# Kernel optimization log

Hardware: AMD Instinct MI355X
Metric: run time of the kernel (lower is better)

## Reference

```python
import jax, jax.numpy as jnp
import numpy as np

B, T, H = 16, 512, 384   # batch, phoneme length, hidden
F, K = 384, 3            # filter size, kernel size
DMAX = 8                 # max per-token duration
L = T * DMAX             # static max expanded length (original uses real_len.max())


def conv1d_same(x, w, b):
    # x: [B, T, Cin], w: [Cout, Cin, K] (torch OIW layout), padding = K//2 both sides
    y = jax.lax.conv_general_dilated(
        x.transpose(0, 2, 1), w, window_strides=(1,),
        padding=[(K // 2, K // 2)], dimension_numbers=('NCW', 'OIW', 'NCW'))
    return y.transpose(0, 2, 1) + b


def layer_norm(x, g, b, eps=1e-5):
    mu = jnp.mean(x, axis=-1, keepdims=True)
    var = jnp.mean(jnp.square(x - mu), axis=-1, keepdims=True)
    return (x - mu) * jax.lax.rsqrt(var + eps) * g + b


def setup_inputs() -> dict:
    key = jax.random.key(0)
    ks = jax.random.split(key, 10)
    x = jax.random.normal(ks[0], (B, T, H), dtype=jnp.float32)
    # log-durations whose exp().round() gives integers in [1, DMAX]
    dur = jax.random.randint(ks[1], (B, T), 1, DMAX + 1)
    true_durations = jnp.log(dur.astype(jnp.float32))
    s1 = 1.0 / np.sqrt(H * K)
    s2 = 1.0 / np.sqrt(F * K)
    s3 = 1.0 / np.sqrt(F)
    return {
        'x': x,
        'true_durations': true_durations,
        'conv1_w': jax.random.uniform(ks[2], (F, H, K), jnp.float32, -s1, s1),
        'conv1_b': jnp.zeros((F,), jnp.float32),
        'ln1_g': jnp.ones((F,), jnp.float32),
        'ln1_b': jnp.zeros((F,), jnp.float32),
        'conv2_w': jax.random.uniform(ks[3], (F, F, K), jnp.float32, -s2, s2),
        'conv2_b': jnp.zeros((F,), jnp.float32),
        'ln2_g': jnp.ones((F,), jnp.float32),
        'ln2_b': jnp.zeros((F,), jnp.float32),
        'lin_w': jax.random.uniform(ks[4], (F, 1), jnp.float32, -s3, s3),
        'lin_b': jnp.zeros((1,), jnp.float32),
    }


def reference(x, true_durations, conv1_w, conv1_b, ln1_g, ln1_b,
              conv2_w, conv2_b, ln2_g, ln2_b, lin_w, lin_b):
    # duration predictor net (dropout in eval mode = identity)
    h = conv1d_same(x, conv1_w, conv1_b)
    h = jax.nn.gelu(layer_norm(h, ln1_g, ln1_b), approximate=False)
    h = conv1d_same(h, conv2_w, conv2_b)
    h = jax.nn.gelu(layer_norm(h, ln2_g, ln2_b), approximate=False)
    length = jax.nn.relu(h @ lin_w + lin_b)[..., 0]  # [B, T]

    # length regulation with ground-truth durations (detached ints in original)
    dur = jnp.round(jnp.exp(true_durations)).astype(jnp.int32)  # [B, T]
    ends = jnp.cumsum(dur, axis=1)          # [B, T]
    starts = ends - dur                     # [B, T]
    k = jnp.arange(L)                       # [L]
    # binary alignment: A[b,t,l] = 1 iff starts[b,t] <= l < ends[b,t]
    A = ((k >= starts[..., None]) & (k < ends[..., None])).astype(x.dtype)  # [B,T,L]
    out = jnp.einsum('bth,btl->blh', x, A)  # = (x^T @ A)^T, [B, L, H]
    return out, length
```

## Files before the change

### kernel.cpp

```cpp
#include <hip/hip_runtime.h>
#include <stdint.h>

typedef unsigned short u16;
typedef unsigned int   u32;

#define B_    16
#define T_    512
#define H_    384
#define F_    384
#define DMAX_ 8
#define L_    4096
#define KD    1152
#define M_    8192

typedef __bf16 bf16x8 __attribute__((ext_vector_type(8)));
typedef float  f32x4  __attribute__((ext_vector_type(4)));

typedef __attribute__((address_space(1))) u32 gu32;
typedef __attribute__((address_space(3))) u32 lu32;

__device__ __forceinline__ void dma16(const void* g, void* l) {
    __builtin_amdgcn_global_load_lds((gu32*)(uintptr_t)g, (lu32*)(u32)(uintptr_t)l, 16, 0, 0);
}

__device__ __forceinline__ u16 f2b(float f) {
    union { float f; u32 i; } v; v.f = f;
    u32 x = v.i;
    return (u16)((x + 0x7fffu + ((x >> 16) & 1u)) >> 16);
}

__global__ void k_durmap(const float* __restrict__ td, int* __restrict__ tmap) {
    __shared__ int s[T_];
    int b = blockIdx.x, t = threadIdx.x;
    int d = (int)roundf(expf(td[b * T_ + t]));
    if (d < 0) d = 0; if (d > DMAX_) d = DMAX_;
    int v = d;
    s[t] = v;
    __syncthreads();
    for (int off = 1; off < T_; off <<= 1) {
        int add = (t >= off) ? s[t - off] : 0;
        __syncthreads();
        v += add;
        s[t] = v;
        __syncthreads();
    }
    int end = v, start = end - d;
    for (int i = start; i < end; ++i) tmap[b * L_ + i] = t;
    int total = s[T_ - 1];
    for (int l = total + t; l < L_; l += T_) tmap[b * L_ + l] = -1;
}

__global__ void k_expand(const float* __restrict__ x, const int* __restrict__ tmap,
                         float* __restrict__ out) {
    int v = blockIdx.x * blockDim.x + threadIdx.x;
    if (v >= B_ * L_ * 96) return;
    int row = v / 96, c4 = v % 96;
    int b = row >> 12;
    int t = tmap[row];
    uint4 val = make_uint4(0u, 0u, 0u, 0u);
    if (t >= 0) val = *(const uint4*)(x + (size_t)((b << 9) + t) * H_ + c4 * 4);
    *(uint4*)(out + (size_t)row * H_ + c4 * 4) = val;
}

__global__ void k_xcast(const float* __restrict__ x, u16* __restrict__ xb) {
    int v = blockIdx.x * blockDim.x + threadIdx.x;
    if (v >= M_ * 96) return;
    float4 f = *(const float4*)(x + (size_t)v * 4);
    u16 o[4] = { f2b(f.x), f2b(f.y), f2b(f.z), f2b(f.w) };
    *(uint2*)(xb + (size_t)v * 4) = *(uint2*)o;
}

__global__ void k_repack(const float* __restrict__ w1, const float* __restrict__ w2,
                         u16* __restrict__ Wp1, u16* __restrict__ Wp2,
                         u16* __restrict__ zp) {
    int i = blockIdx.x * blockDim.x + threadIdx.x;
    if (i < 128) zp[i] = 0;
    const int n = F_ * H_ * 3;
    if (i >= 2 * n) return;
    const float* src = (i < n) ? w1 : w2;
    u16* dst         = (i < n) ? Wp1 : Wp2;
    int j = (i < n) ? i : i - n;
    int f = j / (H_ * 3);
    int rem = j % (H_ * 3);
    int c = rem / 3, kk = rem % 3;
    dst[f * KD + kk * H_ + c] = f2b(src[j]);
}

__launch_bounds__(256, 4)
__global__ void k_gemm(const u16* __restrict__ src, const u16* __restrict__ Wp,
                       const float* __restrict__ bias, float* __restrict__ C,
                       const u16* __restrict__ zp) {
    __shared__ u16 smem[768 * 8];
    int tid = threadIdx.x;
    int w = tid >> 6, lane = tid & 63;
    int quad = lane >> 4, l16 = lane & 15;
    int m0 = blockIdx.x * 64;
    int n0 = blockIdx.y * 128;

    int idx0 = w * 64 + lane;
    int rowA = idx0 >> 2;
    int qA   = (idx0 & 3) ^ ((rowA >> 1) & 3);
    int arow = m0 + rowA;
    int bB   = arow >> 9, tt = arow & 511;
    int rowB = idx0 >> 2;
    int qB   = (idx0 & 3) ^ ((rowB >> 1) & 3);
    const u16* srcB1 = Wp + (size_t)(n0 + rowB) * KD + qB * 8;
    const u16* srcB2 = Wp + (size_t)(n0 + rowB + 64) * KD + qB * 8;
    u16* ldsA  = smem + (size_t)w * 512;
    u16* ldsB1 = smem + 2048 + (size_t)w * 512;
    u16* ldsB2 = smem + 4096 + (size_t)w * 512;

    int wm = w & 1, wn = w >> 1;
    const u16* aptr[2];
    const u16* bptr[4];
    #pragma unroll
    for (int i = 0; i < 2; ++i) {
        int row = wm * 32 + i * 16 + l16;
        aptr[i] = smem + (((row << 2) | (quad ^ ((row >> 1) & 3))) << 3);
    }
    #pragma unroll
    for (int j = 0; j < 4; ++j) {
        int row = wn * 64 + j * 16 + l16;
        bptr[j] = smem + ((256 + ((row << 2) | (quad ^ ((row >> 1) & 3)))) << 3);
    }

    f32x4 acc[2][4];
    #pragma unroll
    for (int i = 0; i < 2; ++i)
        #pragma unroll
        for (int j = 0; j < 4; ++j)
            acc[i][j] = f32x4{0.f, 0.f, 0.f, 0.f};

    for (int k0 = 0; k0 < KD; k0 += 32) {
        int kg = k0 + qA * 8;
        int kk = (kg >= 768) ? 2 : ((kg >= 384) ? 1 : 0);
        int c  = kg - kk * 384;
        int ts = tt + kk - 1;
        const u16* sA = (ts >= 0 && ts < T_) ? (src + (size_t)((bB << 9) + ts) * H_ + c) : zp;
        dma16(sA, ldsA);
        dma16(srcB1 + k0, ldsB1);
        dma16(srcB2 + k0, ldsB2);
        __syncthreads();

        bf16x8 af[2], bfr[4];
        #pragma unroll
        for (int i = 0; i < 2; ++i) af[i]  = *(const bf16x8*)aptr[i];
        #pragma unroll
        for (int j = 0; j < 4; ++j) bfr[j] = *(const bf16x8*)bptr[j];
        #pragma unroll
        for (int i = 0; i < 2; ++i)
            #pragma unroll
            for (int j = 0; j < 4; ++j)
                acc[i][j] = __builtin_amdgcn_mfma_f32_16x16x32_bf16(af[i], bfr[j], acc[i][j], 0, 0, 0);
        __syncthreads();
    }

    #pragma unroll
    for (int i = 0; i < 2; ++i) {
        #pragma unroll
        for (int j = 0; j < 4; ++j) {
            int row = m0 + wm * 32 + i * 16 + quad * 4;
            int col = n0 + wn * 64 + j * 16 + l16;
            float bb = bias[col];
            #pragma unroll
            for (int r = 0; r < 4; ++r)
                C[(size_t)(row + r) * F_ + col] = acc[i][j][r] + bb;
        }
    }
}

__global__ void k_lngelu(const float* __restrict__ Hin, const float* __restrict__ g,
                         const float* __restrict__ bta, u16* __restrict__ G) {
    int row = blockIdx.x;
    int lane = threadIdx.x;
    const float* hr = Hin + (size_t)row * F_;
    float vals[6];
    float s = 0.f, s2 = 0.f;
    #pragma unroll
    for (int j = 0; j < 6; ++j) {
        float xv = hr[lane + j * 64];
        vals[j] = xv; s += xv; s2 += xv * xv;
    }
    #pragma unroll
    for (int off = 32; off; off >>= 1) { s += __shfl_down(s, off); s2 += __shfl_down(s2, off); }
    s = __shfl(s, 0); s2 = __shfl(s2, 0);
    float mean = s * (1.f / F_);
    float var  = s2 * (1.f / F_) - mean * mean;
    float rstd = rsqrtf(var + 1e-5f);
    #pragma unroll
    for (int j = 0; j < 6; ++j) {
        int c = lane + j * 64;
        float y  = (vals[j] - mean) * rstd * g[c] + bta[c];
        float gl = 0.5f * y * (1.f + erff(y * 0.70710678118654752f));
        G[(size_t)row * F_ + c] = f2b(gl);
    }
}

__global__ void k_len(const float* __restrict__ Hin, const float* __restrict__ g,
                      const float* __restrict__ bta, const float* __restrict__ lw,
                      const float* __restrict__ lb, float* __restrict__ lenout) {
    int row = blockIdx.x;
    int lane = threadIdx.x;
    const float* hr = Hin + (size_t)row * F_;
    float vals[6];
    float s = 0.f, s2 = 0.f;
    #pragma unroll
    for (int j = 0; j < 6; ++j) {
        float xv = hr[lane + j * 64];
        vals[j] = xv; s += xv; s2 += xv * xv;
    }
    #pragma unroll
    for (int off = 32; off; off >>= 1) { s += __shfl_down(s, off); s2 += __shfl_down(s2, off); }
    s = __shfl(s, 0); s2 = __shfl(s2, 0);
    float mean = s * (1.f / F_);
    float var  = s2 * (1.f / F_) - mean * mean;
    float rstd = rsqrtf(var + 1e-5f);
    float dot = 0.f;
    #pragma unroll
    for (int j = 0; j < 6; ++j) {
        int c = lane + j * 64;
        float y  = (vals[j] - mean) * rstd * g[c] + bta[c];
        float gl = 0.5f * y * (1.f + erff(y * 0.70710678118654752f));
        dot += gl * lw[c];
    }
    #pragma unroll
    for (int off = 32; off; off >>= 1) dot += __shfl_down(dot, off);
    if (lane == 0) {
        float r = dot + lb[0];
        lenout[row] = fmaxf(r, 0.f);
    }
}

extern "C" void kernel_launch(void* const* d_in, const int* in_sizes, int n_in,
                              void* d_out, int out_size, void* d_ws, size_t ws_size,
                              hipStream_t stream) {
    const float* x   = (const float*)d_in[0];
    const float* td  = (const float*)d_in[1];
    const float* w1  = (const float*)d_in[2];
    const float* b1  = (const float*)d_in[3];
    const float* g1  = (const float*)d_in[4];
    const float* be1 = (const float*)d_in[5];
    const float* w2  = (const float*)d_in[6];
    const float* b2  = (const float*)d_in[7];
    const float* g2  = (const float*)d_in[8];
    const float* be2 = (const float*)d_in[9];
    const float* lw  = (const float*)d_in[10];
    const float* lb  = (const float*)d_in[11];

    float* out0 = (float*)d_out;
    float* out1 = out0 + (size_t)B_ * L_ * H_;

    char* ws = (char*)d_ws;
    size_t off = 0;
    auto carve = [&](size_t bytes) -> void* {
        void* p = ws + off;
        off = (off + bytes + 255) & ~(size_t)255;
        return p;
    };
    int*  tmap  = (int*)carve((size_t)B_ * L_ * sizeof(int));
    u16*  Wp1   = (u16*)carve((size_t)F_ * KD * sizeof(u16));
    u16*  Wp2   = (u16*)carve((size_t)F_ * KD * sizeof(u16));
    u16*  xb    = (u16*)carve((size_t)M_ * H_ * sizeof(u16));
    u16*  G     = (u16*)carve((size_t)M_ * F_ * sizeof(u16));
    u16*  zp    = (u16*)carve(256);
    float* Hbuf = (float*)carve((size_t)M_ * F_ * sizeof(float));

    k_durmap<<<B_, T_, 0, stream>>>(td, tmap);
    k_expand<<<(B_ * L_ * 96 + 255) / 256, 256, 0, stream>>>(x, tmap, out0);

    k_repack<<<(2 * F_ * H_ * 3 + 255) / 256, 256, 0, stream>>>(w1, w2, Wp1, Wp2, zp);
    k_xcast<<<(M_ * 96 + 255) / 256, 256, 0, stream>>>(x, xb);
    k_gemm<<<dim3(M_ / 64, 3), 256, 0, stream>>>(xb, Wp1, b1, Hbuf, zp);
    k_lngelu<<<M_, 64, 0, stream>>>(Hbuf, g1, be1, G);
    k_gemm<<<dim3(M_ / 64, 3), 256, 0, stream>>>(G, Wp2, b2, Hbuf, zp);
    k_len<<<M_, 64, 0, stream>>>(Hbuf, g2, be2, lw, lb, out1);
}
```

Baseline: 212.0 us.

## Retile conv GEMM to 32x128 with K=64 steps and store bf16 intermediates

The conv GEMM moves from 64x128 tiles with K=32 steps to 32x128 tiles with K=64 steps. This halves the number of barrier pairs and doubles MFMA work per sync, and the grid doubles to 768 blocks. The A-row gather now precomputes three tap base pointers instead of branching per step. The GEMM output is stored as bf16 rather than fp32, halving intermediate traffic into the LayerNorm kernels at the cost of an extra rounding before normalization.

After: 197.9 us. 6.7% less time.

```diff
diff --git a/kernel.cpp b/kernel.cpp
--- a/kernel.cpp
+++ b/kernel.cpp
@@ -27,6 +27,9 @@
     union { float f; u32 i; } v; v.f = f;
     u32 x = v.i;
     return (u16)((x + 0x7fffu + ((x >> 16) & 1u)) >> 16);
+}
+__device__ __forceinline__ float b2f(u16 u) {
+    union { u32 i; float f; } v; v.i = ((u32)u) << 16; return v.f;
 }
 
 __global__ void k_durmap(const float* __restrict__ td, int* __restrict__ tmap) {
@@ -74,7 +77,7 @@
                          u16* __restrict__ Wp1, u16* __restrict__ Wp2,
                          u16* __restrict__ zp) {
     int i = blockIdx.x * blockDim.x + threadIdx.x;
-    if (i < 128) zp[i] = 0;
+    if (i < 512) zp[i] = 0;
     const int n = F_ * H_ * 3;
     if (i >= 2 * n) return;
     const float* src = (i < n) ? w1 : w2;
@@ -86,99 +89,119 @@
     dst[f * KD + kk * H_ + c] = f2b(src[j]);
 }
 
-__launch_bounds__(256, 4)
+__launch_bounds__(256, 3)
 __global__ void k_gemm(const u16* __restrict__ src, const u16* __restrict__ Wp,
-                       const float* __restrict__ bias, float* __restrict__ C,
+                       const float* __restrict__ bias, u16* __restrict__ Hb,
                        const u16* __restrict__ zp) {
-    __shared__ u16 smem[768 * 8];
+    __shared__ u16 smem[1280 * 8];
     int tid = threadIdx.x;
     int w = tid >> 6, lane = tid & 63;
     int quad = lane >> 4, l16 = lane & 15;
-    int m0 = blockIdx.x * 64;
+    int m0 = blockIdx.x * 32;
     int n0 = blockIdx.y * 128;
 
-    int idx0 = w * 64 + lane;
-    int rowA = idx0 >> 2;
-    int qA   = (idx0 & 3) ^ ((rowA >> 1) & 3);
+    int rowA = tid >> 3;
+    int qlA  = (tid & 7) ^ (rowA & 7);
+    int coffA = qlA * 8;
     int arow = m0 + rowA;
-    int bB   = arow >> 9, tt = arow & 511;
-    int rowB = idx0 >> 2;
-    int qB   = (idx0 & 3) ^ ((rowB >> 1) & 3);
-    const u16* srcB1 = Wp + (size_t)(n0 + rowB) * KD + qB * 8;
-    const u16* srcB2 = Wp + (size_t)(n0 + rowB + 64) * KD + qB * 8;
-    u16* ldsA  = smem + (size_t)w * 512;
-    u16* ldsB1 = smem + 2048 + (size_t)w * 512;
-    u16* ldsB2 = smem + 4096 + (size_t)w * 512;
-
-    int wm = w & 1, wn = w >> 1;
-    const u16* aptr[2];
-    const u16* bptr[4];
+    int bB = arow >> 9, tt = arow & 511;
+    const u16* abase[3];
+    #pragma unroll
+    for (int kk = 0; kk < 3; ++kk) {
+        int ts = tt + kk - 1;
+        abase[kk] = (ts >= 0 && ts < T_) ? (src + (size_t)((bB << 9) + ts) * H_ + coffA)
+                                         : (zp + coffA);
+    }
+    u16* destA = smem + (size_t)w * 512;
+    const u16* bsrc[4];
+    u16* destB[4];
+    #pragma unroll
+    for (int p = 0; p < 4; ++p) {
+        int bc = tid + p * 256;
+        int rowB = bc >> 3;
+        int qlB  = (bc & 7) ^ (rowB & 7);
+        bsrc[p]  = Wp + (size_t)(n0 + rowB) * KD + qlB * 8;
+        destB[p] = smem + (size_t)((p + 1) * 256 + w * 64) * 8;
+    }
+
+    const u16* aptr[2][2];
+    const u16* bptr[2][2];
+    #pragma unroll
+    for (int i = 0; i < 2; ++i)
+        #pragma unroll
+        for (int kv = 0; kv < 2; ++kv) {
+            int row = i * 16 + l16;
+            aptr[i][kv] = smem + (size_t)((row << 3) | ((kv * 4 + quad) ^ (row & 7))) * 8;
+        }
+    #pragma unroll
+    for (int j = 0; j < 2; ++j)
+        #pragma unroll
+        for (int kv = 0; kv < 2; ++kv) {
+            int row = w * 32 + j * 16 + l16;
+            bptr[j][kv] = smem + (size_t)(256 + ((row << 3) | ((kv * 4 + quad) ^ (row & 7)))) * 8;
+        }
+
+    f32x4 acc[2][2];
+    #pragma unroll
+    for (int i = 0; i < 2; ++i)
+        #pragma unroll
+        for (int j = 0; j < 2; ++j)
+            acc[i][j] = f32x4{0.f, 0.f, 0.f, 0.f};
+
+    #pragma unroll
+    for (int kk = 0; kk < 3; ++kk) {
+        #pragma unroll
+        for (int s = 0; s < 6; ++s) {
+            int k0 = kk * 384 + s * 64;
+            dma16(abase[kk] + s * 64, destA);
+            #pragma unroll
+            for (int p = 0; p < 4; ++p) dma16(bsrc[p] + k0, destB[p]);
+            __syncthreads();
+
+            bf16x8 af[2][2], bf[2][2];
+            #pragma unroll
+            for (int i = 0; i < 2; ++i)
+                #pragma unroll
+                for (int kv = 0; kv < 2; ++kv) af[i][kv] = *(const bf16x8*)aptr[i][kv];
+            #pragma unroll
+            for (int j = 0; j < 2; ++j)
+                #pragma unroll
+                for (int kv = 0; kv < 2; ++kv) bf[j][kv] = *(const bf16x8*)bptr[j][kv];
+            #pragma unroll
+            for (int kv = 0; kv < 2; ++kv)
+                #pragma unroll
+                for (int i = 0; i < 2; ++i)
+                    #pragma unroll
+                    for (int j = 0; j < 2; ++j)
+                        acc[i][j] = __builtin_amdgcn_mfma_f32_16x16x32_bf16(af[i][kv], bf[j][kv], acc[i][j], 0, 0, 0);
+            __syncthreads();
+        }
+    }
+
     #pragma unroll
     for (int i = 0; i < 2; ++i) {
-        int row = wm * 32 + i * 16 + l16;
-        aptr[i] = smem + (((row << 2) | (quad ^ ((row >> 1) & 3))) << 3);
-    }
-    #pragma unroll
-    for (int j = 0; j < 4; ++j) {
-        int row = wn * 64 + j * 16 + l16;
-        bptr[j] = smem + ((256 + ((row << 2) | (quad ^ ((row >> 1) & 3)))) << 3);
-    }
-
-    f32x4 acc[2][4];
-    #pragma unroll
-    for (int i = 0; i < 2; ++i)
-        #pragma unroll
-        for (int j = 0; j < 4; ++j)
-            acc[i][j] = f32x4{0.f, 0.f, 0.f, 0.f};
-
-    for (int k0 = 0; k0 < KD; k0 += 32) {
-        int kg = k0 + qA * 8;
-        int kk = (kg >= 768) ? 2 : ((kg >= 384) ? 1 : 0);
-        int c  = kg - kk * 384;
-        int ts = tt + kk - 1;
-        const u16* sA = (ts >= 0 && ts < T_) ? (src + (size_t)((bB << 9) + ts) * H_ + c) : zp;
-        dma16(sA, ldsA);
-        dma16(srcB1 + k0, ldsB1);
-        dma16(srcB2 + k0, ldsB2);
-        __syncthreads();
-
-        bf16x8 af[2], bfr[4];
-        #pragma unroll
-        for (int i = 0; i < 2; ++i) af[i]  = *(const bf16x8*)aptr[i];
-        #pragma unroll
-        for (int j = 0; j < 4; ++j) bfr[j] = *(const bf16x8*)bptr[j];
-        #pragma unroll
-        for (int i = 0; i < 2; ++i)
-            #pragma unroll
-            for (int j = 0; j < 4; ++j)
-                acc[i][j] = __builtin_amdgcn_mfma_f32_16x16x32_bf16(af[i], bfr[j], acc[i][j], 0, 0, 0);
-        __syncthreads();
-    }
-
-    #pragma unroll
-    for (int i = 0; i < 2; ++i) {
-        #pragma unroll
-        for (int j = 0; j < 4; ++j) {
-            int row = m0 + wm * 32 + i * 16 + quad * 4;
-            int col = n0 + wn * 64 + j * 16 + l16;
+        #pragma unroll
+        for (int j = 0; j < 2; ++j) {
+            int row = m0 + i * 16 + quad * 4;
+            int col = n0 + w * 32 + j * 16 + l16;
             float bb = bias[col];
             #pragma unroll
             for (int r = 0; r < 4; ++r)
-                C[(size_t)(row + r) * F_ + col] = acc[i][j][r] + bb;
+                Hb[(size_t)(row + r) * F_ + col] = f2b(acc[i][j][r] + bb);
         }
     }
 }
 
-__global__ void k_lngelu(const float* __restrict__ Hin, const float* __restrict__ g,
+__global__ void k_lngelu(const u16* __restrict__ Hin, const float* __restrict__ g,
                          const float* __restrict__ bta, u16* __restrict__ G) {
     int row = blockIdx.x;
     int lane = threadIdx.x;
-    const float* hr = Hin + (size_t)row * F_;
+    const u16* hr = Hin + (size_t)row * F_;
     float vals[6];
     float s = 0.f, s2 = 0.f;
     #pragma unroll
     for (int j = 0; j < 6; ++j) {
-        float xv = hr[lane + j * 64];
+        float xv = b2f(hr[lane + j * 64]);
         vals[j] = xv; s += xv; s2 += xv * xv;
     }
     #pragma unroll
@@ -196,17 +219,17 @@
     }
 }
 
-__global__ void k_len(const float* __restrict__ Hin, const float* __restrict__ g,
+__global__ void k_len(const u16* __restrict__ Hin, const float* __restrict__ g,
                       const float* __restrict__ bta, const float* __restrict__ lw,
                       const float* __restrict__ lb, float* __restrict__ lenout) {
     int row = blockIdx.x;
     int lane = threadIdx.x;
-    const float* hr = Hin + (size_t)row * F_;
+    const u16* hr = Hin + (size_t)row * F_;
     float vals[6];
     float s = 0.f, s2 = 0.f;
     #pragma unroll
     for (int j = 0; j < 6; ++j) {
-        float xv = hr[lane + j * 64];
+        float xv = b2f(hr[lane + j * 64]);
         vals[j] = xv; s += xv; s2 += xv * xv;
     }
     #pragma unroll
@@ -257,21 +280,21 @@
         off = (off + bytes + 255) & ~(size_t)255;
         return p;
     };
-    int*  tmap  = (int*)carve((size_t)B_ * L_ * sizeof(int));
-    u16*  Wp1   = (u16*)carve((size_t)F_ * KD * sizeof(u16));
-    u16*  Wp2   = (u16*)carve((size_t)F_ * KD * sizeof(u16));
-    u16*  xb    = (u16*)carve((size_t)M_ * H_ * sizeof(u16));
-    u16*  G     = (u16*)carve((size_t)M_ * F_ * sizeof(u16));
-    u16*  zp    = (u16*)carve(256);
-    float* Hbuf = (float*)carve((size_t)M_ * F_ * sizeof(float));
+    int*  tmap = (int*)carve((size_t)B_ * L_ * sizeof(int));
+    u16*  Wp1  = (u16*)carve((size_t)F_ * KD * sizeof(u16));
+    u16*  Wp2  = (u16*)carve((size_t)F_ * KD * sizeof(u16));
+    u16*  xb   = (u16*)carve((size_t)M_ * H_ * sizeof(u16));
+    u16*  G    = (u16*)carve((size_t)M_ * F_ * sizeof(u16));
+    u16*  zp   = (u16*)carve(1024);
+    u16*  Hb   = (u16*)carve((size_t)M_ * F_ * sizeof(u16));
 
     k_durmap<<<B_, T_, 0, stream>>>(td, tmap);
     k_expand<<<(B_ * L_ * 96 + 255) / 256, 256, 0, stream>>>(x, tmap, out0);
 
     k_repack<<<(2 * F_ * H_ * 3 + 255) / 256, 256, 0, stream>>>(w1, w2, Wp1, Wp2, zp);
     k_xcast<<<(M_ * 96 + 255) / 256, 256, 0, stream>>>(x, xb);
-    k_gemm<<<dim3(M_ / 64, 3), 256, 0, stream>>>(xb, Wp1, b1, Hbuf, zp);
-    k_lngelu<<<M_, 64, 0, stream>>>(Hbuf, g1, be1, G);
-    k_gemm<<<dim3(M_ / 64, 3), 256, 0, stream>>>(G, Wp2, b2, Hbuf, zp);
-    k_len<<<M_, 64, 0, stream>>>(Hbuf, g2, be2, lw, lb, out1);
-}
+    k_gemm<<<dim3(M_ / 32, 3), 256, 0, stream>>>(xb, Wp1, b1, Hb, zp);
+    k_lngelu<<<M_, 64, 0, stream>>>(Hb, g1, be1, G);
+    k_gemm<<<dim3(M_ / 32, 3), 256, 0, stream>>>(G, Wp2, b2, Hb, zp);
+    k_len<<<M_, 64, 0, stream>>>(Hb, g2, be2, lw, lb, out1);
+}
```
